# Kernel tuning notes

Measured on AMD Instinct MI355X. Metric: run time of the kernel, lower is better.

Reference implementation:

```python
import jax, jax.numpy as jnp
import numpy as np
import math

B, N = 1, 768
C1, C2 = 384, 128
H, SQK, SV, PQK, PV, NC = 12, 16, 16, 4, 8, 384
EPS = 1e-8
SCALAR_W = math.sqrt(1.0 / (3.0 * SQK))           # sqrt(1/(num_logit_terms*scalar_variance))
POINT_W = math.sqrt(1.0 / (3.0 * (PQK * 9.0 / 2.0)))
W2D = math.sqrt(1.0 / 3.0)


def _quat_to_rot(q):
    # q: [..., 4] -> orthonormal rotation matrices [..., 3, 3]
    q = q / jnp.linalg.norm(q, axis=-1, keepdims=True)
    w, x, y, z = q[..., 0], q[..., 1], q[..., 2], q[..., 3]
    r0 = jnp.stack([1 - 2 * (y * y + z * z), 2 * (x * y - w * z), 2 * (x * z + w * y)], -1)
    r1 = jnp.stack([2 * (x * y + w * z), 1 - 2 * (x * x + z * z), 2 * (y * z - w * x)], -1)
    r2 = jnp.stack([2 * (x * z - w * y), 2 * (y * z + w * x), 1 - 2 * (x * x + y * y)], -1)
    return jnp.stack([r0, r1, r2], -2)


def setup_inputs() -> dict:
    key = jax.random.key(0)
    ks = jax.random.split(key, 12)

    def lin(k, o, i):
        kw, kb = jax.random.split(k)
        w = jax.random.normal(kw, (o, i), jnp.float32) / np.sqrt(i).astype(np.float32)
        b = jax.random.normal(kb, (o,), jnp.float32) * 0.01
        return w, b

    w_qs, b_qs = lin(ks[0], H * SQK, C1)
    w_kvs, b_kvs = lin(ks[1], H * (SV + SQK), C1)
    w_qp, b_qp = lin(ks[2], H * 3 * PQK, C1)
    w_kvp, b_kvp = lin(ks[3], H * 3 * (PQK + PV), C1)
    w_a2, b_a2 = lin(ks[4], H, C2)
    w_o, b_o = lin(ks[5], NC, H * (C2 + SV + 4 * PV))
    return {
        'inputs_1d': jax.random.normal(ks[6], (B, N, C1), jnp.float32),
        'inputs_2d': jax.random.normal(ks[7], (B, N, N, C2), jnp.float32),
        'mask': jnp.ones((B, N, 1), jnp.float32),
        'rotation': _quat_to_rot(jax.random.normal(ks[8], (B, N, 4), jnp.float32)),
        'translation': jax.random.normal(ks[9], (B, N, 3), jnp.float32) * 10.0,
        'w_q_scalar': w_qs, 'b_q_scalar': b_qs,
        'w_kv_scalar': w_kvs, 'b_kv_scalar': b_kvs,
        'w_q_point': w_qp, 'b_q_point': b_qp,
        'w_kv_point': w_kvp, 'b_kv_point': b_kvp,
        'tpw': jnp.ones((H,), jnp.float32),
        'w_attn2d': w_a2, 'b_attn2d': b_a2,
        'w_out': w_o, 'b_out': b_o,
    }


def ipa_forward(inputs_1d, inputs_2d, mask, rotation, translation,
                w_q_scalar, b_q_scalar, w_kv_scalar, b_kv_scalar,
                w_q_point, b_q_point, w_kv_point, b_kv_point,
                tpw, w_attn2d, b_attn2d, w_out, b_out):
    Bs, Ns, _ = inputs_1d.shape

    # scalar q/k/v
    q_scalar = (inputs_1d @ w_q_scalar.T + b_q_scalar).reshape(Bs, Ns, H, SQK)
    kv_scalar = (inputs_1d @ w_kv_scalar.T + b_kv_scalar).reshape(Bs, Ns, H, SQK + SV)
    k_scalar, v_scalar = kv_scalar[..., :SQK], kv_scalar[..., SQK:]

    # point q/k/v in local frame; split order is 3 coord chunks of size H*P
    qp = (inputs_1d @ w_q_point.T + b_q_point).reshape(Bs, Ns, 3, H * PQK)
    kvp = (inputs_1d @ w_kv_point.T + b_kv_point).reshape(Bs, Ns, 3, H * (PQK + PV))
    # to global frame: p_global = R @ p_local + t
    qg = jnp.einsum('bnij,bnjm->bnim', rotation, qp) + translation[..., None]
    kvg = jnp.einsum('bnij,bnjm->bnim', rotation, kvp) + translation[..., None]
    q_point = qg.reshape(Bs, Ns, 3, H, PQK).transpose(0, 3, 1, 4, 2)          # [B,H,N,Pqk,3]
    kv_point = kvg.reshape(Bs, Ns, 3, H, PQK + PV).transpose(0, 3, 1, 4, 2)    # [B,H,N,Pqk+Pv,3]
    k_point, v_point = kv_point[..., :PQK, :], kv_point[..., PQK:, :]

    # point-distance attention term: sum_{p,c} (q-k)^2 = |q|^2 + |k|^2 - 2 q.k
    pw = jax.nn.softplus(tpw) * POINT_W                                       # [H]
    qn = jnp.sum(q_point * q_point, axis=(-1, -2))                             # [B,H,N]
    kn = jnp.sum(k_point * k_point, axis=(-1, -2))
    qk = jnp.einsum('bhipc,bhjpc->bhij', q_point, k_point)
    dist2 = qn[..., :, None] + kn[..., None, :] - 2.0 * qk                     # [B,H,N,N]
    attn_qk_point = -0.5 * pw[None, :, None, None] * dist2

    # scalar attention term
    attn_qk_scalar = jnp.einsum('bihd,bjhd->bhij', SCALAR_W * q_scalar, k_scalar)

    # pair-bias term
    a2d = inputs_2d @ w_attn2d.T + b_attn2d                                    # [B,N,N,H]
    logits = attn_qk_scalar + attn_qk_point + W2D * a2d.transpose(0, 3, 1, 2)

    mask2d = mask * jnp.swapaxes(mask, -1, -2)                                 # [B,N,N]
    logits = logits - 1e5 * (1.0 - mask2d[:, None, :, :])
    attn = jax.nn.softmax(logits, axis=-1)                                     # [B,H,N,N]

    # scalar values
    result_scalar = jnp.einsum('bhij,bjhd->bihd', attn, v_scalar).reshape(Bs, Ns, H * SV)

    # point values (global), then back to local frame: p_local = R^T (p - t)
    rpg = jnp.einsum('bhij,bhjpc->bhipc', attn, v_point)                       # [B,H,N,Pv,3]
    rpg = rpg.transpose(0, 2, 4, 1, 3).reshape(Bs, Ns, 3, H * PV)              # [B,N,3,M]
    local = jnp.einsum('bnji,bnjm->bnim', rotation, rpg - translation[..., None])
    dist = jnp.sqrt(EPS + jnp.sum(local * local, axis=2))                      # [B,N,M]

    # attention over pair features
    r2d = jnp.einsum('bhij,bijc->bihc', attn, inputs_2d).reshape(Bs, Ns, H * C2)

    final_act = jnp.concatenate(
        [result_scalar, local[:, :, 0], local[:, :, 1], local[:, :, 2], dist, r2d], axis=-1)
    return final_act @ w_out.T + b_out


def reference(inputs_1d, inputs_2d, mask, rotation, translation,
              w_q_scalar, b_q_scalar, w_kv_scalar, b_kv_scalar,
              w_q_point, b_q_point, w_kv_point, b_kv_point,
              tpw, w_attn2d, b_attn2d, w_out, b_out):
    return ipa_forward(inputs_1d, inputs_2d, mask, rotation, translation,
                       w_q_scalar, b_q_scalar, w_kv_scalar, b_kv_scalar,
                       w_q_point, b_q_point, w_kv_point, b_kv_point,
                       tpw, w_attn2d, b_attn2d, w_out, b_out)
```

## Files before the change

kernel.cpp:

```cpp
#include <hip/hip_runtime.h>
#include <hip/hip_bf16.h>
#include <math.h>

#define NRES 768
#define C1 384
#define C2 128
#define NH 12

#define OFF_QS   0
#define OFF_KS   147456
#define OFF_VS   294912
#define OFF_QPT  442368
#define OFF_KPT  552960
#define OFF_VPT  663552
#define OFF_FA   884736
#define OFF_RAW  OFF_FA

__device__ __forceinline__ float dot4(float4 a, float4 b) {
    return fmaf(a.x, b.x, fmaf(a.y, b.y, fmaf(a.z, b.z, a.w * b.w)));
}

static constexpr float SCALAR_W = 0.14433756729740643f;
static constexpr float POINT_W  = 0.13608276348795434f;
static constexpr float W2D_W    = 0.57735026918962576f;

__device__ __forceinline__ void wsel(int o,
    const float* w_qs, const float* b_qs, const float* w_kvs, const float* b_kvs,
    const float* w_qp, const float* b_qp, const float* w_kvp, const float* b_kvp,
    const float** row, float* bias)
{
    if (o < 192)      { *row = w_qs  + (size_t)o * C1;         *bias = b_qs[o]; }
    else if (o < 576) { *row = w_kvs + (size_t)(o - 192) * C1; *bias = b_kvs[o - 192]; }
    else if (o < 720) { *row = w_qp  + (size_t)(o - 576) * C1; *bias = b_qp[o - 576]; }
    else              { *row = w_kvp + (size_t)(o - 720) * C1; *bias = b_kvp[o - 720]; }
}

__global__ __launch_bounds__(256) void k1_gemm(
    const float* __restrict__ in1d,
    const float* __restrict__ w_qs, const float* __restrict__ b_qs,
    const float* __restrict__ w_kvs, const float* __restrict__ b_kvs,
    const float* __restrict__ w_qp, const float* __restrict__ b_qp,
    const float* __restrict__ w_kvp, const float* __restrict__ b_kvp,
    float* __restrict__ ws)
{
    __shared__ __align__(16) float ASt[32][68];
    __shared__ __align__(16) float WSt[32][68];
    const int t = threadIdx.x;
    const int n0 = blockIdx.x * 64;
    const int o0 = blockIdx.y * 64;
    const int tx = t & 15, ty = t >> 4;
    float acc[4][4];
    #pragma unroll
    for (int r = 0; r < 4; ++r)
        #pragma unroll
        for (int c = 0; c < 4; ++c) acc[r][c] = 0.f;

    for (int k0 = 0; k0 < C1; k0 += 32) {
        __syncthreads();
        #pragma unroll
        for (int s = 0; s < 2; ++s) {
            int q = t + 256 * s;
            int row = q >> 3, kq = (q & 7) * 4;
            float4 a4 = *(const float4*)&in1d[(size_t)(n0 + row) * C1 + k0 + kq];
            ASt[kq + 0][row] = a4.x; ASt[kq + 1][row] = a4.y;
            ASt[kq + 2][row] = a4.z; ASt[kq + 3][row] = a4.w;
            const float* wr; float bb;
            wsel(o0 + row, w_qs, b_qs, w_kvs, b_kvs, w_qp, b_qp, w_kvp, b_kvp, &wr, &bb);
            float4 w4 = *(const float4*)&wr[k0 + kq];
            WSt[kq + 0][row] = w4.x; WSt[kq + 1][row] = w4.y;
            WSt[kq + 2][row] = w4.z; WSt[kq + 3][row] = w4.w;
        }
        __syncthreads();
        #pragma unroll
        for (int k = 0; k < 32; ++k) {
            float4 a4 = *(const float4*)&ASt[k][ty * 4];
            float4 w4 = *(const float4*)&WSt[k][tx * 4];
            float av[4] = {a4.x, a4.y, a4.z, a4.w};
            float wv[4] = {w4.x, w4.y, w4.z, w4.w};
            #pragma unroll
            for (int r = 0; r < 4; ++r)
                #pragma unroll
                for (int c = 0; c < 4; ++c)
                    acc[r][c] = fmaf(av[r], wv[c], acc[r][c]);
        }
    }
    float bias[4];
    #pragma unroll
    for (int c = 0; c < 4; ++c) {
        const float* dummy;
        wsel(o0 + tx * 4 + c, w_qs, b_qs, w_kvs, b_kvs, w_qp, b_qp, w_kvp, b_kvp, &dummy, &bias[c]);
    }
    float* raw = ws + OFF_RAW;
    #pragma unroll
    for (int r = 0; r < 4; ++r) {
        int n = n0 + ty * 4 + r;
        *(float4*)&raw[(size_t)n * 1152 + o0 + tx * 4] =
            make_float4(acc[r][0] + bias[0], acc[r][1] + bias[1],
                        acc[r][2] + bias[2], acc[r][3] + bias[3]);
    }
}

__global__ __launch_bounds__(256) void k1b_scatter(
    const float* __restrict__ rot, const float* __restrict__ trans,
    float* __restrict__ ws)
{
    __shared__ __align__(16) float rawS[1152];
    const int t = threadIdx.x;
    const int i = blockIdx.x;
    const float* raw = ws + OFF_RAW + (size_t)i * 1152;
    for (int q = t; q < 288; q += 256) *(float4*)&rawS[q * 4] = *(const float4*)&raw[q * 4];
    __syncthreads();
    float* qs  = ws + OFF_QS;  float* ks  = ws + OFF_KS;  float* vs  = ws + OFF_VS;
    float* qpt = ws + OFF_QPT; float* kpt = ws + OFF_KPT; float* vpt = ws + OFF_VPT;

    for (int o = t; o < 576; o += 256) {
        float v = rawS[o];
        if (o < 192) {
            qs[(size_t)i * 192 + o] = v * SCALAR_W;
        } else {
            int idx = o - 192, h = idx >> 5, d = idx & 31;
            if (d < 16) ks[(size_t)i * 192 + h * 16 + d] = v;
            else        vs[(size_t)i * 192 + h * 16 + (d - 16)] = v;
        }
    }
    if (t < 192) {
        int m = t;
        float x0, x1, x2;
        if (m < 48) { x0 = rawS[576 + m]; x1 = rawS[624 + m]; x2 = rawS[672 + m]; }
        else { int mm = m - 48; x0 = rawS[720 + mm]; x1 = rawS[864 + mm]; x2 = rawS[1008 + mm]; }
        float g[3];
        #pragma unroll
        for (int ii = 0; ii < 3; ++ii)
            g[ii] = rot[i * 9 + ii * 3 + 0] * x0 + rot[i * 9 + ii * 3 + 1] * x1 +
                    rot[i * 9 + ii * 3 + 2] * x2 + trans[i * 3 + ii];
        if (m < 48) {
            #pragma unroll
            for (int ii = 0; ii < 3; ++ii) qpt[(size_t)i * 144 + 3 * m + ii] = g[ii];
        } else {
            int mm = m - 48, h = mm / 12, pp = mm % 12;
            if (pp < 4) {
                #pragma unroll
                for (int ii = 0; ii < 3; ++ii) kpt[(size_t)i * 144 + h * 12 + pp * 3 + ii] = g[ii];
            } else {
                #pragma unroll
                for (int ii = 0; ii < 3; ++ii) vpt[(size_t)i * 288 + h * 24 + (pp - 4) * 3 + ii] = g[ii];
            }
        }
    }
}

#define TJ 256
__global__ __launch_bounds__(256) void k2_attn(
    const float* __restrict__ in2d,
    const float* __restrict__ mask,
    const float* __restrict__ rot, const float* __restrict__ trans,
    const float* __restrict__ tpw,
    const float* __restrict__ w2d, const float* __restrict__ b2d,
    float* __restrict__ ws)
{
    __shared__ __align__(16) float P[NH][264];
    __shared__ __align__(16) float tileS[64][128];
    __shared__ __align__(16) float qsS[192];
    __shared__ __align__(16) float qptS[144];
    __shared__ float qnS[NH], phS[NH], bbS[NH], mS[NH], lS[NH], aS[NH];
    __shared__ float rpgS[288];
    const int t = threadIdx.x;
    const int i = blockIdx.x;

    const float* qs  = ws + OFF_QS;  const float* ks  = ws + OFF_KS;  const float* vs = ws + OFF_VS;
    const float* qpt = ws + OFF_QPT; const float* kpt = ws + OFF_KPT; const float* vpt = ws + OFF_VPT;

    if (t < 48) *(float4*)&qsS[t * 4] = *(const float4*)&qs[(size_t)i * 192 + t * 4];
    else if (t >= 64 && t < 100) { int u = t - 64; *(float4*)&qptS[u * 4] = *(const float4*)&qpt[(size_t)i * 144 + u * 4]; }
    __syncthreads();
    if (t < NH) {
        float s = 0.f;
        #pragma unroll
        for (int e = 0; e < 12; ++e) { float x = qptS[t * 12 + e]; s += x * x; }
        qnS[t] = s;
        phS[t] = -0.5f * POINT_W * logf(1.f + __expf(tpw[t]));
        bbS[t] = W2D_W * b2d[t];
        mS[t] = -1e30f;
        lS[t] = 0.f;
    }
    __syncthreads();
    const float mi = mask[i];

    float ra[4] = {0.f, 0.f, 0.f, 0.f};
    float rb[4] = {0.f, 0.f, 0.f, 0.f};
    const bool isR2 = (t < 192);
    int h0 = 0, h1 = 0, c4 = 0, o0 = 0, vh = 0;
    const float* vbase = nullptr; int vstride = 0; bool vact = false;
    if (isR2) { h0 = (t >> 5) * 2; h1 = h0 + 1; c4 = t & 31; }
    else {
        int u = t - 192; o0 = u * 8; vact = (u < 60);
        if (vact) {
            if (o0 < 192) { vh = o0 >> 4; vbase = vs + o0; vstride = 192; }
            else { int q0 = o0 - 192; vh = q0 / 24; vbase = vpt + q0; vstride = 288; }
        }
    }

    for (int tile = 0; tile < 3; ++tile) {
        const int j0 = tile * TJ;
        __syncthreads();
        {
            const int j = j0 + t;
            float acc[NH];
            #pragma unroll
            for (int h = 0; h < NH; ++h) acc[h] = 0.f;
            const float* row = in2d + ((size_t)i * NRES + j) * C2;
            #pragma unroll 8
            for (int cc = 0; cc < 32; ++cc) {
                float4 v4 = *(const float4*)&row[cc * 4];
                #pragma unroll
                for (int h = 0; h < NH; ++h) {
                    float4 w4 = *(const float4*)&w2d[h * C2 + cc * 4];
                    acc[h] += dot4(v4, w4);
                }
            }
            const float msub = -100000.0f * (1.0f - mi * mask[j]);
            const float* ksr  = ks  + (size_t)j * 192;
            const float* kptr = kpt + (size_t)j * 144;
            #pragma unroll
            for (int h = 0; h < NH; ++h) {
                float sq = 0.f;
                #pragma unroll
                for (int d4 = 0; d4 < 4; ++d4) {
                    float4 q4 = *(const float4*)&qsS[h * 16 + d4 * 4];
                    float4 k4 = *(const float4*)&ksr[h * 16 + d4 * 4];
                    sq += dot4(q4, k4);
                }
                float qk = 0.f, kk = 0.f;
                #pragma unroll
                for (int e4 = 0; e4 < 3; ++e4) {
                    float4 qp4 = *(const float4*)&qptS[h * 12 + e4 * 4];
                    float4 kp4 = *(const float4*)&kptr[h * 12 + e4 * 4];
                    qk += dot4(qp4, kp4);
                    kk += dot4(kp4, kp4);
                }
                P[h][t] = sq + phS[h] * (qnS[h] + kk - 2.f * qk) + W2D_W * acc[h] + bbS[h] + msub;
            }
        }
        __syncthreads();
        {
            int wv = t >> 6, lane = t & 63;
            for (int h = wv * 3; h < wv * 3 + 3; ++h) {
                float v0 = P[h][lane], v1 = P[h][lane + 64], v2 = P[h][lane + 128], v3 = P[h][lane + 192];
                float mt = fmaxf(fmaxf(v0, v1), fmaxf(v2, v3));
                #pragma unroll
                for (int off = 32; off > 0; off >>= 1) mt = fmaxf(mt, __shfl_xor(mt, off));
                float mold = mS[h];
                float mnew = fmaxf(mold, mt);
                float e0 = __expf(v0 - mnew), e1 = __expf(v1 - mnew);
                float e2 = __expf(v2 - mnew), e3 = __expf(v3 - mnew);
                P[h][lane] = e0; P[h][lane + 64] = e1; P[h][lane + 128] = e2; P[h][lane + 192] = e3;
                float s = e0 + e1 + e2 + e3;
                #pragma unroll
                for (int off = 32; off > 0; off >>= 1) s += __shfl_xor(s, off);
                if (lane == 0) {
                    float a = __expf(mold - mnew);
                    aS[h] = a;
                    lS[h] = lS[h] * a + s;
                    mS[h] = mnew;
                }
            }
        }
        __syncthreads();
        if (isR2) {
            float a0 = aS[h0], a1 = aS[h1];
            #pragma unroll
            for (int k = 0; k < 4; ++k) { ra[k] *= a0; rb[k] *= a1; }
        } else if (vact) {
            float a = aS[vh];
            #pragma unroll
            for (int k = 0; k < 4; ++k) { ra[k] *= a; rb[k] *= a; }
        }
        for (int sub = 0; sub < 4; ++sub) {
            __syncthreads();
            #pragma unroll
            for (int s = 0; s < 8; ++s) {
                int q = t + 256 * s;
                int rr = q >> 5, cc = q & 31;
                *(float4*)&tileS[rr][cc * 4] =
                    *(const float4*)&in2d[((size_t)i * NRES + j0 + sub * 64 + rr) * C2 + cc * 4];
            }
            __syncthreads();
            if (isR2) {
                for (int jj = 0; jj < 64; jj += 4) {
                    int jt = sub * 64 + jj;
                    float4 p0 = *(const float4*)&P[h0][jt];
                    float4 p1 = *(const float4*)&P[h1][jt];
                    float w0[4] = {p0.x, p0.y, p0.z, p0.w};
                    float w1[4] = {p1.x, p1.y, p1.z, p1.w};
                    #pragma unroll
                    for (int k = 0; k < 4; ++k) {
                        float4 v4 = *(const float4*)&tileS[jj + k][c4 * 4];
                        ra[0] = fmaf(w0[k], v4.x, ra[0]); ra[1] = fmaf(w0[k], v4.y, ra[1]);
                        ra[2] = fmaf(w0[k], v4.z, ra[2]); ra[3] = fmaf(w0[k], v4.w, ra[3]);
                        rb[0] = fmaf(w1[k], v4.x, rb[0]); rb[1] = fmaf(w1[k], v4.y, rb[1]);
                        rb[2] = fmaf(w1[k], v4.z, rb[2]); rb[3] = fmaf(w1[k], v4.w, rb[3]);
                    }
                }
            } else if (vact) {
                for (int jj = 0; jj < 64; jj += 4) {
                    int jt = sub * 64 + jj;
                    int jg = j0 + jt;
                    float4 p = *(const float4*)&P[vh][jt];
                    float w[4] = {p.x, p.y, p.z, p.w};
                    #pragma unroll
                    for (int k = 0; k < 4; ++k) {
                        float4 va = *(const float4*)&vbase[(size_t)(jg + k) * vstride];
                        float4 vb = *(const float4*)&vbase[(size_t)(jg + k) * vstride + 4];
                        ra[0] = fmaf(w[k], va.x, ra[0]); ra[1] = fmaf(w[k], va.y, ra[1]);
                        ra[2] = fmaf(w[k], va.z, ra[2]); ra[3] = fmaf(w[k], va.w, ra[3]);
                        rb[0] = fmaf(w[k], vb.x, rb[0]); rb[1] = fmaf(w[k], vb.y, rb[1]);
                        rb[2] = fmaf(w[k], vb.z, rb[2]); rb[3] = fmaf(w[k], vb.w, rb[3]);
                    }
                }
            }
        }
    }
    float* fa = ws + OFF_FA + (size_t)i * 2112;
    if (isR2) {
        float n0v = 1.f / lS[h0], n1v = 1.f / lS[h1];
        *(float4*)&fa[576 + h0 * 128 + c4 * 4] = make_float4(ra[0] * n0v, ra[1] * n0v, ra[2] * n0v, ra[3] * n0v);
        *(float4*)&fa[576 + h1 * 128 + c4 * 4] = make_float4(rb[0] * n1v, rb[1] * n1v, rb[2] * n1v, rb[3] * n1v);
    } else if (vact) {
        float nv = 1.f / lS[vh];
        if (o0 < 192) {
            *(float4*)&fa[o0]     = make_float4(ra[0] * nv, ra[1] * nv, ra[2] * nv, ra[3] * nv);
            *(float4*)&fa[o0 + 4] = make_float4(rb[0] * nv, rb[1] * nv, rb[2] * nv, rb[3] * nv);
        } else {
            int q0 = o0 - 192;
            *(float4*)&rpgS[q0]     = make_float4(ra[0] * nv, ra[1] * nv, ra[2] * nv, ra[3] * nv);
            *(float4*)&rpgS[q0 + 4] = make_float4(rb[0] * nv, rb[1] * nv, rb[2] * nv, rb[3] * nv);
        }
    }
    __syncthreads();
    if (t < 96) {
        int h = t >> 3, p = t & 7;
        float rv[3];
        #pragma unroll
        for (int c = 0; c < 3; ++c) rv[c] = rpgS[h * 24 + p * 3 + c] - trans[i * 3 + c];
        float l0 = rot[i * 9 + 0] * rv[0] + rot[i * 9 + 3] * rv[1] + rot[i * 9 + 6] * rv[2];
        float l1 = rot[i * 9 + 1] * rv[0] + rot[i * 9 + 4] * rv[1] + rot[i * 9 + 7] * rv[2];
        float l2 = rot[i * 9 + 2] * rv[0] + rot[i * 9 + 5] * rv[1] + rot[i * 9 + 8] * rv[2];
        float dd = sqrtf(1e-8f + l0 * l0 + l1 * l1 + l2 * l2);
        fa[192 + t] = l0;
        fa[288 + t] = l1;
        fa[384 + t] = l2;
        fa[480 + t] = dd;
    }
}

__global__ __launch_bounds__(256) void k3_out(
    const float* __restrict__ w_out, const float* __restrict__ b_out,
    const float* __restrict__ ws, float* __restrict__ out)
{
    __shared__ __align__(16) float ASt[32][34];
    __shared__ __align__(16) float WSt[32][34];
    const int t = threadIdx.x;
    const int i0 = blockIdx.x * 32;
    const int o0 = blockIdx.y * 32;
    const float* fa = ws + OFF_FA;
    int tx = t & 15, ty = t >> 4;
    float acc00 = 0.f, acc01 = 0.f, acc10 = 0.f, acc11 = 0.f;
    int r = t >> 3, kq = (t & 7) * 4;

    for (int k0 = 0; k0 < 2112; k0 += 32) {
        __syncthreads();
        {
            float4 a4 = *(const float4*)&fa[(size_t)(i0 + r) * 2112 + k0 + kq];
            ASt[kq + 0][r] = a4.x; ASt[kq + 1][r] = a4.y; ASt[kq + 2][r] = a4.z; ASt[kq + 3][r] = a4.w;
            float4 w4 = *(const float4*)&w_out[(size_t)(o0 + r) * 2112 + k0 + kq];
            WSt[kq + 0][r] = w4.x; WSt[kq + 1][r] = w4.y; WSt[kq + 2][r] = w4.z; WSt[kq + 3][r] = w4.w;
        }
        __syncthreads();
        #pragma unroll
        for (int k = 0; k < 32; ++k) {
            float2 av = *(const float2*)&ASt[k][ty * 2];
            float2 wv = *(const float2*)&WSt[k][tx * 2];
            acc00 = fmaf(av.x, wv.x, acc00);
            acc01 = fmaf(av.x, wv.y, acc01);
            acc10 = fmaf(av.y, wv.x, acc10);
            acc11 = fmaf(av.y, wv.y, acc11);
        }
    }
    int oi = i0 + ty * 2, oo = o0 + tx * 2;
    out[(size_t)oi * 384 + oo]           = acc00 + b_out[oo];
    out[(size_t)oi * 384 + oo + 1]       = acc01 + b_out[oo + 1];
    out[(size_t)(oi + 1) * 384 + oo]     = acc10 + b_out[oo];
    out[(size_t)(oi + 1) * 384 + oo + 1] = acc11 + b_out[oo + 1];
}

extern "C" void kernel_launch(void* const* d_in, const int* in_sizes, int n_in,
                              void* d_out, int out_size, void* d_ws, size_t ws_size,
                              hipStream_t stream) {
    const float* in1d  = (const float*)d_in[0];
    const float* in2d  = (const float*)d_in[1];
    const float* mask  = (const float*)d_in[2];
    const float* rot   = (const float*)d_in[3];
    const float* trans = (const float*)d_in[4];
    const float* w_qs  = (const float*)d_in[5];
    const float* b_qs  = (const float*)d_in[6];
    const float* w_kvs = (const float*)d_in[7];
    const float* b_kvs = (const float*)d_in[8];
    const float* w_qp  = (const float*)d_in[9];
    const float* b_qp  = (const float*)d_in[10];
    const float* w_kvp = (const float*)d_in[11];
    const float* b_kvp = (const float*)d_in[12];
    const float* tpw   = (const float*)d_in[13];
    const float* w2d   = (const float*)d_in[14];
    const float* b2d   = (const float*)d_in[15];
    const float* w_out = (const float*)d_in[16];
    const float* b_out = (const float*)d_in[17];
    float* ws  = (float*)d_ws;
    float* out = (float*)d_out;

    hipLaunchKernelGGL(k1_gemm, dim3(12, 18), dim3(256), 0, stream,
                       in1d, w_qs, b_qs, w_kvs, b_kvs, w_qp, b_qp, w_kvp, b_kvp, ws);
    hipLaunchKernelGGL(k1b_scatter, dim3(768), dim3(256), 0, stream,
                       rot, trans, ws);
    hipLaunchKernelGGL(k2_attn, dim3(768), dim3(256), 0, stream,
                       in2d, mask, rot, trans, tpw, w2d, b2d, ws);
    hipLaunchKernelGGL(k3_out, dim3(24, 12), dim3(256), 0, stream,
                       w_out, b_out, ws, out);
}
```

Measured before the change: 702.3 us.

## Read pair features once per tile with register prefetch and per-wave softmax

The attention kernel now handles 64-key tiles. Each tile of pair features is loaded into shared memory once and reused for both the 2D logit projection and the weighted pair-feature sum, where before the row was read twice from global memory. The next tile is prefetched into registers while the current one is consumed. Each wave computes logits and the online softmax for three heads, with no separate softmax pass. The output GEMM also gets register double-buffering of its global loads. The cost is more tile iterations and barriers, and a smaller key tile per softmax rescale.

```diff
diff --git a/kernel.cpp b/kernel.cpp
--- a/kernel.cpp
+++ b/kernel.cpp
@@ -149,7 +149,7 @@
     }
 }
 
-#define TJ 256
+#define TJ2 64
 __global__ __launch_bounds__(256) void k2_attn(
     const float* __restrict__ in2d,
     const float* __restrict__ mask,
@@ -158,8 +158,8 @@
     const float* __restrict__ w2d, const float* __restrict__ b2d,
     float* __restrict__ ws)
 {
-    __shared__ __align__(16) float P[NH][264];
-    __shared__ __align__(16) float tileS[64][128];
+    __shared__ __align__(16) float tileS[64][132];
+    __shared__ __align__(16) float P[NH][68];
     __shared__ __align__(16) float qsS[192];
     __shared__ __align__(16) float qptS[144];
     __shared__ float qnS[NH], phS[NH], bbS[NH], mS[NH], lS[NH], aS[NH];
@@ -183,15 +183,16 @@
         mS[t] = -1e30f;
         lS[t] = 0.f;
     }
-    __syncthreads();
     const float mi = mask[i];
 
-    float ra[4] = {0.f, 0.f, 0.f, 0.f};
-    float rb[4] = {0.f, 0.f, 0.f, 0.f};
+    const int jrow = t >> 2, p = t & 3;
+    const int lane = t & 63;
+    const int wv = __builtin_amdgcn_readfirstlane(t >> 6);
+    const int h0w = wv * 3;
     const bool isR2 = (t < 192);
-    int h0 = 0, h1 = 0, c4 = 0, o0 = 0, vh = 0;
+    int h0p = 0, h1p = 0, c4 = 0, o0 = 0, vh = 0;
     const float* vbase = nullptr; int vstride = 0; bool vact = false;
-    if (isR2) { h0 = (t >> 5) * 2; h1 = h0 + 1; c4 = t & 31; }
+    if (isR2) { h0p = (t >> 5) * 2; h1p = h0p + 1; c4 = t & 31; }
     else {
         int u = t - 192; o0 = u * 8; vact = (u < 60);
         if (vact) {
@@ -200,96 +201,90 @@
         }
     }
 
-    for (int tile = 0; tile < 3; ++tile) {
-        const int j0 = tile * TJ;
+    float ra[4] = {0.f, 0.f, 0.f, 0.f};
+    float rb[4] = {0.f, 0.f, 0.f, 0.f};
+
+    float4 r[8];
+    {
+        const float* nr = in2d + ((size_t)i * NRES + jrow) * C2 + p * 32;
+        #pragma unroll
+        for (int k = 0; k < 8; ++k) r[k] = *(const float4*)&nr[k * 4];
+    }
+
+    for (int tile = 0; tile < 12; ++tile) {
+        const int j0 = tile * TJ2;
+        __syncthreads();
+        #pragma unroll
+        for (int k = 0; k < 8; ++k) *(float4*)&tileS[jrow][p * 32 + k * 4] = r[k];
         __syncthreads();
         {
-            const int j = j0 + t;
-            float acc[NH];
+            const int j = j0 + lane;
+            const float* ksr  = ks  + (size_t)j * 192 + h0w * 16;
+            const float* kptr = kpt + (size_t)j * 144 + h0w * 12;
+            const float msub = -100000.0f * (1.0f - mi * mask[j]);
+            const float* wrow = w2d + h0w * C2;
+            float a0 = 0.f, a1 = 0.f, a2 = 0.f;
             #pragma unroll
-            for (int h = 0; h < NH; ++h) acc[h] = 0.f;
-            const float* row = in2d + ((size_t)i * NRES + j) * C2;
-            #pragma unroll 8
-            for (int cc = 0; cc < 32; ++cc) {
-                float4 v4 = *(const float4*)&row[cc * 4];
-                #pragma unroll
-                for (int h = 0; h < NH; ++h) {
-                    float4 w4 = *(const float4*)&w2d[h * C2 + cc * 4];
-                    acc[h] += dot4(v4, w4);
-                }
+            for (int c = 0; c < 32; ++c) {
+                float4 v4 = *(const float4*)&tileS[lane][c * 4];
+                a0 += dot4(v4, *(const float4*)&wrow[c * 4]);
+                a1 += dot4(v4, *(const float4*)&wrow[C2 + c * 4]);
+                a2 += dot4(v4, *(const float4*)&wrow[2 * C2 + c * 4]);
             }
-            const float msub = -100000.0f * (1.0f - mi * mask[j]);
-            const float* ksr  = ks  + (size_t)j * 192;
-            const float* kptr = kpt + (size_t)j * 144;
+            float lg[3];
             #pragma unroll
-            for (int h = 0; h < NH; ++h) {
+            for (int e = 0; e < 3; ++e) {
+                int h = h0w + e;
                 float sq = 0.f;
                 #pragma unroll
-                for (int d4 = 0; d4 < 4; ++d4) {
-                    float4 q4 = *(const float4*)&qsS[h * 16 + d4 * 4];
-                    float4 k4 = *(const float4*)&ksr[h * 16 + d4 * 4];
-                    sq += dot4(q4, k4);
-                }
+                for (int d4 = 0; d4 < 4; ++d4)
+                    sq += dot4(*(const float4*)&qsS[h * 16 + d4 * 4],
+                               *(const float4*)&ksr[e * 16 + d4 * 4]);
                 float qk = 0.f, kk = 0.f;
                 #pragma unroll
                 for (int e4 = 0; e4 < 3; ++e4) {
+                    float4 kp4 = *(const float4*)&kptr[e * 12 + e4 * 4];
                     float4 qp4 = *(const float4*)&qptS[h * 12 + e4 * 4];
-                    float4 kp4 = *(const float4*)&kptr[h * 12 + e4 * 4];
                     qk += dot4(qp4, kp4);
                     kk += dot4(kp4, kp4);
                 }
-                P[h][t] = sq + phS[h] * (qnS[h] + kk - 2.f * qk) + W2D_W * acc[h] + bbS[h] + msub;
+                float a2d = (e == 0) ? a0 : ((e == 1) ? a1 : a2);
+                lg[e] = sq + phS[h] * (qnS[h] + kk - 2.f * qk) + W2D_W * a2d + bbS[h] + msub;
             }
-        }
-        __syncthreads();
-        {
-            int wv = t >> 6, lane = t & 63;
-            for (int h = wv * 3; h < wv * 3 + 3; ++h) {
-                float v0 = P[h][lane], v1 = P[h][lane + 64], v2 = P[h][lane + 128], v3 = P[h][lane + 192];
-                float mt = fmaxf(fmaxf(v0, v1), fmaxf(v2, v3));
+            #pragma unroll
+            for (int e = 0; e < 3; ++e) {
+                int h = h0w + e;
+                float mt = lg[e];
                 #pragma unroll
                 for (int off = 32; off > 0; off >>= 1) mt = fmaxf(mt, __shfl_xor(mt, off));
                 float mold = mS[h];
                 float mnew = fmaxf(mold, mt);
-                float e0 = __expf(v0 - mnew), e1 = __expf(v1 - mnew);
-                float e2 = __expf(v2 - mnew), e3 = __expf(v3 - mnew);
-                P[h][lane] = e0; P[h][lane + 64] = e1; P[h][lane + 128] = e2; P[h][lane + 192] = e3;
-                float s = e0 + e1 + e2 + e3;
+                float ev = __expf(lg[e] - mnew);
+                P[h][lane] = ev;
+                float s = ev;
                 #pragma unroll
                 for (int off = 32; off > 0; off >>= 1) s += __shfl_xor(s, off);
                 if (lane == 0) {
-                    float a = __expf(mold - mnew);
-                    aS[h] = a;
-                    lS[h] = lS[h] * a + s;
+                    float al = __expf(mold - mnew);
+                    aS[h] = al;
+                    lS[h] = lS[h] * al + s;
                     mS[h] = mnew;
                 }
             }
         }
         __syncthreads();
-        if (isR2) {
-            float a0 = aS[h0], a1 = aS[h1];
-            #pragma unroll
-            for (int k = 0; k < 4; ++k) { ra[k] *= a0; rb[k] *= a1; }
-        } else if (vact) {
-            float a = aS[vh];
-            #pragma unroll
-            for (int k = 0; k < 4; ++k) { ra[k] *= a; rb[k] *= a; }
-        }
-        for (int sub = 0; sub < 4; ++sub) {
-            __syncthreads();
-            #pragma unroll
-            for (int s = 0; s < 8; ++s) {
-                int q = t + 256 * s;
-                int rr = q >> 5, cc = q & 31;
-                *(float4*)&tileS[rr][cc * 4] =
-                    *(const float4*)&in2d[((size_t)i * NRES + j0 + sub * 64 + rr) * C2 + cc * 4];
-            }
-            __syncthreads();
+        {
+            int nt = (tile < 11) ? tile + 1 : 11;
+            const float* nr = in2d + ((size_t)i * NRES + nt * TJ2 + jrow) * C2 + p * 32;
             if (isR2) {
+                float al0 = aS[h0p], al1 = aS[h1p];
+                #pragma unroll
+                for (int k = 0; k < 4; ++k) { ra[k] *= al0; rb[k] *= al1; }
+                #pragma unroll
+                for (int k = 0; k < 8; ++k) r[k] = *(const float4*)&nr[k * 4];
                 for (int jj = 0; jj < 64; jj += 4) {
-                    int jt = sub * 64 + jj;
-                    float4 p0 = *(const float4*)&P[h0][jt];
-                    float4 p1 = *(const float4*)&P[h1][jt];
+                    float4 p0 = *(const float4*)&P[h0p][jj];
+                    float4 p1 = *(const float4*)&P[h1p][jj];
                     float w0[4] = {p0.x, p0.y, p0.z, p0.w};
                     float w1[4] = {p1.x, p1.y, p1.z, p1.w};
                     #pragma unroll
@@ -301,20 +296,26 @@
                         rb[2] = fmaf(w1[k], v4.z, rb[2]); rb[3] = fmaf(w1[k], v4.w, rb[3]);
                     }
                 }
-            } else if (vact) {
-                for (int jj = 0; jj < 64; jj += 4) {
-                    int jt = sub * 64 + jj;
-                    int jg = j0 + jt;
-                    float4 p = *(const float4*)&P[vh][jt];
-                    float w[4] = {p.x, p.y, p.z, p.w};
+            } else {
+                #pragma unroll
+                for (int k = 0; k < 8; ++k) r[k] = *(const float4*)&nr[k * 4];
+                if (vact) {
+                    float al = aS[vh];
                     #pragma unroll
-                    for (int k = 0; k < 4; ++k) {
-                        float4 va = *(const float4*)&vbase[(size_t)(jg + k) * vstride];
-                        float4 vb = *(const float4*)&vbase[(size_t)(jg + k) * vstride + 4];
-                        ra[0] = fmaf(w[k], va.x, ra[0]); ra[1] = fmaf(w[k], va.y, ra[1]);
-                        ra[2] = fmaf(w[k], va.z, ra[2]); ra[3] = fmaf(w[k], va.w, ra[3]);
-                        rb[0] = fmaf(w[k], vb.x, rb[0]); rb[1] = fmaf(w[k], vb.y, rb[1]);
-                        rb[2] = fmaf(w[k], vb.z, rb[2]); rb[3] = fmaf(w[k], vb.w, rb[3]);
+                    for (int k = 0; k < 4; ++k) { ra[k] *= al; rb[k] *= al; }
+                    for (int jj = 0; jj < 64; jj += 4) {
+                        int jg = j0 + jj;
+                        float4 pv = *(const float4*)&P[vh][jj];
+                        float w[4] = {pv.x, pv.y, pv.z, pv.w};
+                        #pragma unroll
+                        for (int k = 0; k < 4; ++k) {
+                            float4 va = *(const float4*)&vbase[(size_t)(jg + k) * vstride];
+                            float4 vb = *(const float4*)&vbase[(size_t)(jg + k) * vstride + 4];
+                            ra[0] = fmaf(w[k], va.x, ra[0]); ra[1] = fmaf(w[k], va.y, ra[1]);
+                            ra[2] = fmaf(w[k], va.z, ra[2]); ra[3] = fmaf(w[k], va.w, ra[3]);
+                            rb[0] = fmaf(w[k], vb.x, rb[0]); rb[1] = fmaf(w[k], vb.y, rb[1]);
+                            rb[2] = fmaf(w[k], vb.z, rb[2]); rb[3] = fmaf(w[k], vb.w, rb[3]);
+                        }
                     }
                 }
             }
@@ -322,9 +323,9 @@
     }
     float* fa = ws + OFF_FA + (size_t)i * 2112;
     if (isR2) {
-        float n0v = 1.f / lS[h0], n1v = 1.f / lS[h1];
-        *(float4*)&fa[576 + h0 * 128 + c4 * 4] = make_float4(ra[0] * n0v, ra[1] * n0v, ra[2] * n0v, ra[3] * n0v);
-        *(float4*)&fa[576 + h1 * 128 + c4 * 4] = make_float4(rb[0] * n1v, rb[1] * n1v, rb[2] * n1v, rb[3] * n1v);
+        float n0v = 1.f / lS[h0p], n1v = 1.f / lS[h1p];
+        *(float4*)&fa[576 + h0p * 128 + c4 * 4] = make_float4(ra[0] * n0v, ra[1] * n0v, ra[2] * n0v, ra[3] * n0v);
+        *(float4*)&fa[576 + h1p * 128 + c4 * 4] = make_float4(rb[0] * n1v, rb[1] * n1v, rb[2] * n1v, rb[3] * n1v);
     } else if (vact) {
         float nv = 1.f / lS[vh];
         if (o0 < 192) {
@@ -338,10 +339,10 @@
     }
     __syncthreads();
     if (t < 96) {
-        int h = t >> 3, p = t & 7;
+        int h = t >> 3, pp = t & 7;
         float rv[3];
         #pragma unroll
-        for (int c = 0; c < 3; ++c) rv[c] = rpgS[h * 24 + p * 3 + c] - trans[i * 3 + c];
+        for (int c = 0; c < 3; ++c) rv[c] = rpgS[h * 24 + pp * 3 + c] - trans[i * 3 + c];
         float l0 = rot[i * 9 + 0] * rv[0] + rot[i * 9 + 3] * rv[1] + rot[i * 9 + 6] * rv[2];
         float l1 = rot[i * 9 + 1] * rv[0] + rot[i * 9 + 4] * rv[1] + rot[i * 9 + 7] * rv[2];
         float l2 = rot[i * 9 + 2] * rv[0] + rot[i * 9 + 5] * rv[1] + rot[i * 9 + 8] * rv[2];
@@ -366,16 +367,19 @@
     int tx = t & 15, ty = t >> 4;
     float acc00 = 0.f, acc01 = 0.f, acc10 = 0.f, acc11 = 0.f;
     int r = t >> 3, kq = (t & 7) * 4;
+    const float* arow = fa + (size_t)(i0 + r) * 2112 + kq;
+    const float* wrow = w_out + (size_t)(o0 + r) * 2112 + kq;
+    float4 a4 = *(const float4*)&arow[0];
+    float4 w4 = *(const float4*)&wrow[0];
 
     for (int k0 = 0; k0 < 2112; k0 += 32) {
-        __syncthreads();
-        {
-            float4 a4 = *(const float4*)&fa[(size_t)(i0 + r) * 2112 + k0 + kq];
-            ASt[kq + 0][r] = a4.x; ASt[kq + 1][r] = a4.y; ASt[kq + 2][r] = a4.z; ASt[kq + 3][r] = a4.w;
-            float4 w4 = *(const float4*)&w_out[(size_t)(o0 + r) * 2112 + k0 + kq];
-            WSt[kq + 0][r] = w4.x; WSt[kq + 1][r] = w4.y; WSt[kq + 2][r] = w4.z; WSt[kq + 3][r] = w4.w;
-        }
-        __syncthreads();
+        ASt[kq + 0][r] = a4.x; ASt[kq + 1][r] = a4.y; ASt[kq + 2][r] = a4.z; ASt[kq + 3][r] = a4.w;
+        WSt[kq + 0][r] = w4.x; WSt[kq + 1][r] = w4.y; WSt[kq + 2][r] = w4.z; WSt[kq + 3][r] = w4.w;
+        __syncthreads();
+        if (k0 + 32 < 2112) {
+            a4 = *(const float4*)&arow[k0 + 32];
+            w4 = *(const float4*)&wrow[k0 + 32];
+        }
         #pragma unroll
         for (int k = 0; k < 32; ++k) {
             float2 av = *(const float2*)&ASt[k][ty * 2];
@@ -385,6 +389,7 @@
             acc10 = fmaf(av.y, wv.x, acc10);
             acc11 = fmaf(av.y, wv.y, acc11);
         }
+        __syncthreads();
     }
     int oi = i0 + ty * 2, oo = o0 + tx * 2;
     out[(size_t)oi * 384 + oo]           = acc00 + b_out[oo];
```

Measured after the change: 972.6 us. 38.5% more time.

## Restructure attention kernel to full-row softmax with 512 threads and split-j accumulation

Applied to the files above, without the earlier changes.

The attention kernel now launches 512 threads and computes logits for all 768 keys up front. It replaces the online (tiled) softmax with a single full-row softmax, so the running max and rescale bookkeeping disappears. Accumulation splits each row across two half-waves over j and combines them with a shuffle. The output GEMM kernel adds register prefetch of the next K tile to overlap global loads with compute. Shared memory for the logits grows, which may limit occupancy.

```diff
diff --git a/kernel.cpp b/kernel.cpp
--- a/kernel.cpp
+++ b/kernel.cpp
@@ -149,8 +149,7 @@
     }
 }
 
-#define TJ 256
-__global__ __launch_bounds__(256) void k2_attn(
+__global__ __launch_bounds__(512, 4) void k2_attn(
     const float* __restrict__ in2d,
     const float* __restrict__ mask,
     const float* __restrict__ rot, const float* __restrict__ trans,
@@ -158,14 +157,16 @@
     const float* __restrict__ w2d, const float* __restrict__ b2d,
     float* __restrict__ ws)
 {
-    __shared__ __align__(16) float P[NH][264];
-    __shared__ __align__(16) float tileS[64][128];
+    __shared__ __align__(16) float P[NH][776];
+    __shared__ __align__(16) float tileS[32][132];
     __shared__ __align__(16) float qsS[192];
     __shared__ __align__(16) float qptS[144];
-    __shared__ float qnS[NH], phS[NH], bbS[NH], mS[NH], lS[NH], aS[NH];
+    __shared__ float qnS[NH], phS[NH], bbS[NH];
     __shared__ float rpgS[288];
     const int t = threadIdx.x;
     const int i = blockIdx.x;
+    const int lane = t & 63;
+    const int wv = t >> 6;
 
     const float* qs  = ws + OFF_QS;  const float* ks  = ws + OFF_KS;  const float* vs = ws + OFF_VS;
     const float* qpt = ws + OFF_QPT; const float* kpt = ws + OFF_KPT; const float* vpt = ws + OFF_VPT;
@@ -180,168 +181,158 @@
         qnS[t] = s;
         phS[t] = -0.5f * POINT_W * logf(1.f + __expf(tpw[t]));
         bbS[t] = W2D_W * b2d[t];
-        mS[t] = -1e30f;
-        lS[t] = 0.f;
     }
     __syncthreads();
     const float mi = mask[i];
 
+    for (int j = t; j < NRES; j += 512) {
+        float acc[NH];
+        #pragma unroll
+        for (int h = 0; h < NH; ++h) acc[h] = 0.f;
+        const float* row = in2d + ((size_t)i * NRES + j) * C2;
+        #pragma unroll 8
+        for (int cc = 0; cc < 32; ++cc) {
+            float4 v4 = *(const float4*)&row[cc * 4];
+            #pragma unroll
+            for (int h = 0; h < NH; ++h) {
+                float4 w4 = *(const float4*)&w2d[h * C2 + cc * 4];
+                acc[h] += dot4(v4, w4);
+            }
+        }
+        const float msub = -100000.0f * (1.0f - mi * mask[j]);
+        const float* ksr  = ks  + (size_t)j * 192;
+        const float* kptr = kpt + (size_t)j * 144;
+        #pragma unroll
+        for (int h = 0; h < NH; ++h) {
+            float sq = 0.f;
+            #pragma unroll
+            for (int d4 = 0; d4 < 4; ++d4) {
+                float4 q4 = *(const float4*)&qsS[h * 16 + d4 * 4];
+                float4 k4 = *(const float4*)&ksr[h * 16 + d4 * 4];
+                sq += dot4(q4, k4);
+            }
+            float qk = 0.f, kk = 0.f;
+            #pragma unroll
+            for (int e4 = 0; e4 < 3; ++e4) {
+                float4 qp4 = *(const float4*)&qptS[h * 12 + e4 * 4];
+                float4 kp4 = *(const float4*)&kptr[h * 12 + e4 * 4];
+                qk += dot4(qp4, kp4);
+                kk += dot4(kp4, kp4);
+            }
+            P[h][j] = sq + phS[h] * (qnS[h] + kk - 2.f * qk) + W2D_W * acc[h] + bbS[h] + msub;
+        }
+    }
+    __syncthreads();
+
+    for (int h = wv; h < NH; h += 8) {
+        float v[12];
+        float mx = -1e30f;
+        #pragma unroll
+        for (int k = 0; k < 12; ++k) { v[k] = P[h][lane + 64 * k]; mx = fmaxf(mx, v[k]); }
+        #pragma unroll
+        for (int off = 32; off > 0; off >>= 1) mx = fmaxf(mx, __shfl_xor(mx, off));
+        float s = 0.f;
+        #pragma unroll
+        for (int k = 0; k < 12; ++k) { v[k] = __expf(v[k] - mx); s += v[k]; }
+        #pragma unroll
+        for (int off = 32; off > 0; off >>= 1) s += __shfl_xor(s, off);
+        float rinv = 1.0f / s;
+        #pragma unroll
+        for (int k = 0; k < 12; ++k) P[h][lane + 64 * k] = v[k] * rinv;
+    }
+    __syncthreads();
+
+    const int jh = lane >> 5;
+    const int c4 = lane & 31;
     float ra[4] = {0.f, 0.f, 0.f, 0.f};
     float rb[4] = {0.f, 0.f, 0.f, 0.f};
-    const bool isR2 = (t < 192);
-    int h0 = 0, h1 = 0, c4 = 0, o0 = 0, vh = 0;
+    int h0 = 0, h1 = 0, vh = 0, vo0 = 0;
     const float* vbase = nullptr; int vstride = 0; bool vact = false;
-    if (isR2) { h0 = (t >> 5) * 2; h1 = h0 + 1; c4 = t & 31; }
+    if (wv < 6) { h0 = wv * 2; h1 = h0 + 1; }
     else {
-        int u = t - 192; o0 = u * 8; vact = (u < 60);
+        int l = lane & 31;
+        vact = (l < 30);
+        vo0 = 240 * (wv - 6) + l * 8;
         if (vact) {
-            if (o0 < 192) { vh = o0 >> 4; vbase = vs + o0; vstride = 192; }
-            else { int q0 = o0 - 192; vh = q0 / 24; vbase = vpt + q0; vstride = 288; }
-        }
-    }
-
-    for (int tile = 0; tile < 3; ++tile) {
-        const int j0 = tile * TJ;
+            if (vo0 < 192) { vh = vo0 >> 4; vbase = vs + vo0; vstride = 192; }
+            else { int q0 = vo0 - 192; vh = q0 / 24; vbase = vpt + q0; vstride = 288; }
+        }
+    }
+
+    for (int sub = 0; sub < 24; ++sub) {
         __syncthreads();
         {
-            const int j = j0 + t;
-            float acc[NH];
-            #pragma unroll
-            for (int h = 0; h < NH; ++h) acc[h] = 0.f;
-            const float* row = in2d + ((size_t)i * NRES + j) * C2;
-            #pragma unroll 8
-            for (int cc = 0; cc < 32; ++cc) {
-                float4 v4 = *(const float4*)&row[cc * 4];
+            int rr = t >> 4, cq = (t & 15) * 8;
+            const float* src = &in2d[((size_t)i * NRES + sub * 32 + rr) * C2 + cq];
+            float4 x0 = *(const float4*)&src[0];
+            float4 x1 = *(const float4*)&src[4];
+            *(float4*)&tileS[rr][cq] = x0;
+            *(float4*)&tileS[rr][cq + 4] = x1;
+        }
+        __syncthreads();
+        const int jbase = sub * 32 + jh * 16;
+        const int jloc = jh * 16;
+        if (wv < 6) {
+            #pragma unroll
+            for (int jj = 0; jj < 16; jj += 4) {
+                float4 p0 = *(const float4*)&P[h0][jbase + jj];
+                float4 p1 = *(const float4*)&P[h1][jbase + jj];
+                float w0[4] = {p0.x, p0.y, p0.z, p0.w};
+                float w1[4] = {p1.x, p1.y, p1.z, p1.w};
                 #pragma unroll
-                for (int h = 0; h < NH; ++h) {
-                    float4 w4 = *(const float4*)&w2d[h * C2 + cc * 4];
-                    acc[h] += dot4(v4, w4);
+                for (int k = 0; k < 4; ++k) {
+                    float4 v4 = *(const float4*)&tileS[jloc + jj + k][c4 * 4];
+                    ra[0] = fmaf(w0[k], v4.x, ra[0]); ra[1] = fmaf(w0[k], v4.y, ra[1]);
+                    ra[2] = fmaf(w0[k], v4.z, ra[2]); ra[3] = fmaf(w0[k], v4.w, ra[3]);
+                    rb[0] = fmaf(w1[k], v4.x, rb[0]); rb[1] = fmaf(w1[k], v4.y, rb[1]);
+                    rb[2] = fmaf(w1[k], v4.z, rb[2]); rb[3] = fmaf(w1[k], v4.w, rb[3]);
                 }
             }
-            const float msub = -100000.0f * (1.0f - mi * mask[j]);
-            const float* ksr  = ks  + (size_t)j * 192;
-            const float* kptr = kpt + (size_t)j * 144;
-            #pragma unroll
-            for (int h = 0; h < NH; ++h) {
-                float sq = 0.f;
+        } else if (vact) {
+            #pragma unroll
+            for (int jj = 0; jj < 16; jj += 4) {
+                float4 pv = *(const float4*)&P[vh][jbase + jj];
+                float w[4] = {pv.x, pv.y, pv.z, pv.w};
                 #pragma unroll
-                for (int d4 = 0; d4 < 4; ++d4) {
-                    float4 q4 = *(const float4*)&qsS[h * 16 + d4 * 4];
-                    float4 k4 = *(const float4*)&ksr[h * 16 + d4 * 4];
-                    sq += dot4(q4, k4);
+                for (int k = 0; k < 4; ++k) {
+                    float4 va = *(const float4*)&vbase[(size_t)(jbase + jj + k) * vstride];
+                    float4 vb = *(const float4*)&vbase[(size_t)(jbase + jj + k) * vstride + 4];
+                    ra[0] = fmaf(w[k], va.x, ra[0]); ra[1] = fmaf(w[k], va.y, ra[1]);
+                    ra[2] = fmaf(w[k], va.z, ra[2]); ra[3] = fmaf(w[k], va.w, ra[3]);
+                    rb[0] = fmaf(w[k], vb.x, rb[0]); rb[1] = fmaf(w[k], vb.y, rb[1]);
+                    rb[2] = fmaf(w[k], vb.z, rb[2]); rb[3] = fmaf(w[k], vb.w, rb[3]);
                 }
-                float qk = 0.f, kk = 0.f;
-                #pragma unroll
-                for (int e4 = 0; e4 < 3; ++e4) {
-                    float4 qp4 = *(const float4*)&qptS[h * 12 + e4 * 4];
-                    float4 kp4 = *(const float4*)&kptr[h * 12 + e4 * 4];
-                    qk += dot4(qp4, kp4);
-                    kk += dot4(kp4, kp4);
-                }
-                P[h][t] = sq + phS[h] * (qnS[h] + kk - 2.f * qk) + W2D_W * acc[h] + bbS[h] + msub;
-            }
-        }
-        __syncthreads();
-        {
-            int wv = t >> 6, lane = t & 63;
-            for (int h = wv * 3; h < wv * 3 + 3; ++h) {
-                float v0 = P[h][lane], v1 = P[h][lane + 64], v2 = P[h][lane + 128], v3 = P[h][lane + 192];
-                float mt = fmaxf(fmaxf(v0, v1), fmaxf(v2, v3));
-                #pragma unroll
-                for (int off = 32; off > 0; off >>= 1) mt = fmaxf(mt, __shfl_xor(mt, off));
-                float mold = mS[h];
-                float mnew = fmaxf(mold, mt);
-                float e0 = __expf(v0 - mnew), e1 = __expf(v1 - mnew);
-                float e2 = __expf(v2 - mnew), e3 = __expf(v3 - mnew);
-                P[h][lane] = e0; P[h][lane + 64] = e1; P[h][lane + 128] = e2; P[h][lane + 192] = e3;
-                float s = e0 + e1 + e2 + e3;
-                #pragma unroll
-                for (int off = 32; off > 0; off >>= 1) s += __shfl_xor(s, off);
-                if (lane == 0) {
-                    float a = __expf(mold - mnew);
-                    aS[h] = a;
-                    lS[h] = lS[h] * a + s;
-                    mS[h] = mnew;
-                }
-            }
-        }
-        __syncthreads();
-        if (isR2) {
-            float a0 = aS[h0], a1 = aS[h1];
-            #pragma unroll
-            for (int k = 0; k < 4; ++k) { ra[k] *= a0; rb[k] *= a1; }
-        } else if (vact) {
-            float a = aS[vh];
-            #pragma unroll
-            for (int k = 0; k < 4; ++k) { ra[k] *= a; rb[k] *= a; }
-        }
-        for (int sub = 0; sub < 4; ++sub) {
-            __syncthreads();
-            #pragma unroll
-            for (int s = 0; s < 8; ++s) {
-                int q = t + 256 * s;
-                int rr = q >> 5, cc = q & 31;
-                *(float4*)&tileS[rr][cc * 4] =
-                    *(const float4*)&in2d[((size_t)i * NRES + j0 + sub * 64 + rr) * C2 + cc * 4];
-            }
-            __syncthreads();
-            if (isR2) {
-                for (int jj = 0; jj < 64; jj += 4) {
-                    int jt = sub * 64 + jj;
-                    float4 p0 = *(const float4*)&P[h0][jt];
-                    float4 p1 = *(const float4*)&P[h1][jt];
-                    float w0[4] = {p0.x, p0.y, p0.z, p0.w};
-                    float w1[4] = {p1.x, p1.y, p1.z, p1.w};
-                    #pragma unroll
-                    for (int k = 0; k < 4; ++k) {
-                        float4 v4 = *(const float4*)&tileS[jj + k][c4 * 4];
-                        ra[0] = fmaf(w0[k], v4.x, ra[0]); ra[1] = fmaf(w0[k], v4.y, ra[1]);
-                        ra[2] = fmaf(w0[k], v4.z, ra[2]); ra[3] = fmaf(w0[k], v4.w, ra[3]);
-                        rb[0] = fmaf(w1[k], v4.x, rb[0]); rb[1] = fmaf(w1[k], v4.y, rb[1]);
-                        rb[2] = fmaf(w1[k], v4.z, rb[2]); rb[3] = fmaf(w1[k], v4.w, rb[3]);
-                    }
-                }
-            } else if (vact) {
-                for (int jj = 0; jj < 64; jj += 4) {
-                    int jt = sub * 64 + jj;
-                    int jg = j0 + jt;
-                    float4 p = *(const float4*)&P[vh][jt];
-                    float w[4] = {p.x, p.y, p.z, p.w};
-                    #pragma unroll
-                    for (int k = 0; k < 4; ++k) {
-                        float4 va = *(const float4*)&vbase[(size_t)(jg + k) * vstride];
-                        float4 vb = *(const float4*)&vbase[(size_t)(jg + k) * vstride + 4];
-                        ra[0] = fmaf(w[k], va.x, ra[0]); ra[1] = fmaf(w[k], va.y, ra[1]);
-                        ra[2] = fmaf(w[k], va.z, ra[2]); ra[3] = fmaf(w[k], va.w, ra[3]);
-                        rb[0] = fmaf(w[k], vb.x, rb[0]); rb[1] = fmaf(w[k], vb.y, rb[1]);
-                        rb[2] = fmaf(w[k], vb.z, rb[2]); rb[3] = fmaf(w[k], vb.w, rb[3]);
-                    }
-                }
-            }
-        }
-    }
+            }
+        }
+    }
+
     float* fa = ws + OFF_FA + (size_t)i * 2112;
-    if (isR2) {
-        float n0v = 1.f / lS[h0], n1v = 1.f / lS[h1];
-        *(float4*)&fa[576 + h0 * 128 + c4 * 4] = make_float4(ra[0] * n0v, ra[1] * n0v, ra[2] * n0v, ra[3] * n0v);
-        *(float4*)&fa[576 + h1 * 128 + c4 * 4] = make_float4(rb[0] * n1v, rb[1] * n1v, rb[2] * n1v, rb[3] * n1v);
-    } else if (vact) {
-        float nv = 1.f / lS[vh];
-        if (o0 < 192) {
-            *(float4*)&fa[o0]     = make_float4(ra[0] * nv, ra[1] * nv, ra[2] * nv, ra[3] * nv);
-            *(float4*)&fa[o0 + 4] = make_float4(rb[0] * nv, rb[1] * nv, rb[2] * nv, rb[3] * nv);
+    #pragma unroll
+    for (int k = 0; k < 4; ++k) {
+        ra[k] += __shfl_xor(ra[k], 32);
+        rb[k] += __shfl_xor(rb[k], 32);
+    }
+    if (wv < 6) {
+        if (lane < 32)
+            *(float4*)&fa[576 + h0 * 128 + c4 * 4] = make_float4(ra[0], ra[1], ra[2], ra[3]);
+        else
+            *(float4*)&fa[576 + h1 * 128 + c4 * 4] = make_float4(rb[0], rb[1], rb[2], rb[3]);
+    } else if (vact && lane < 32) {
+        if (vo0 < 192) {
+            *(float4*)&fa[vo0]     = make_float4(ra[0], ra[1], ra[2], ra[3]);
+            *(float4*)&fa[vo0 + 4] = make_float4(rb[0], rb[1], rb[2], rb[3]);
         } else {
-            int q0 = o0 - 192;
-            *(float4*)&rpgS[q0]     = make_float4(ra[0] * nv, ra[1] * nv, ra[2] * nv, ra[3] * nv);
-            *(float4*)&rpgS[q0 + 4] = make_float4(rb[0] * nv, rb[1] * nv, rb[2] * nv, rb[3] * nv);
+            int q0 = vo0 - 192;
+            *(float4*)&rpgS[q0]     = make_float4(ra[0], ra[1], ra[2], ra[3]);
+            *(float4*)&rpgS[q0 + 4] = make_float4(rb[0], rb[1], rb[2], rb[3]);
         }
     }
     __syncthreads();
     if (t < 96) {
-        int h = t >> 3, p = t & 7;
+        int h = t >> 3, pp = t & 7;
         float rv[3];
         #pragma unroll
-        for (int c = 0; c < 3; ++c) rv[c] = rpgS[h * 24 + p * 3 + c] - trans[i * 3 + c];
+        for (int c = 0; c < 3; ++c) rv[c] = rpgS[h * 24 + pp * 3 + c] - trans[i * 3 + c];
         float l0 = rot[i * 9 + 0] * rv[0] + rot[i * 9 + 3] * rv[1] + rot[i * 9 + 6] * rv[2];
         float l1 = rot[i * 9 + 1] * rv[0] + rot[i * 9 + 4] * rv[1] + rot[i * 9 + 7] * rv[2];
         float l2 = rot[i * 9 + 2] * rv[0] + rot[i * 9 + 5] * rv[1] + rot[i * 9 + 8] * rv[2];
@@ -366,16 +357,19 @@
     int tx = t & 15, ty = t >> 4;
     float acc00 = 0.f, acc01 = 0.f, acc10 = 0.f, acc11 = 0.f;
     int r = t >> 3, kq = (t & 7) * 4;
+    const float* arow = fa + (size_t)(i0 + r) * 2112 + kq;
+    const float* wrow = w_out + (size_t)(o0 + r) * 2112 + kq;
+    float4 a4 = *(const float4*)&arow[0];
+    float4 w4 = *(const float4*)&wrow[0];
 
     for (int k0 = 0; k0 < 2112; k0 += 32) {
-        __syncthreads();
-        {
-            float4 a4 = *(const float4*)&fa[(size_t)(i0 + r) * 2112 + k0 + kq];
-            ASt[kq + 0][r] = a4.x; ASt[kq + 1][r] = a4.y; ASt[kq + 2][r] = a4.z; ASt[kq + 3][r] = a4.w;
-            float4 w4 = *(const float4*)&w_out[(size_t)(o0 + r) * 2112 + k0 + kq];
-            WSt[kq + 0][r] = w4.x; WSt[kq + 1][r] = w4.y; WSt[kq + 2][r] = w4.z; WSt[kq + 3][r] = w4.w;
-        }
-        __syncthreads();
+        ASt[kq + 0][r] = a4.x; ASt[kq + 1][r] = a4.y; ASt[kq + 2][r] = a4.z; ASt[kq + 3][r] = a4.w;
+        WSt[kq + 0][r] = w4.x; WSt[kq + 1][r] = w4.y; WSt[kq + 2][r] = w4.z; WSt[kq + 3][r] = w4.w;
+        __syncthreads();
+        if (k0 + 32 < 2112) {
+            a4 = *(const float4*)&arow[k0 + 32];
+            w4 = *(const float4*)&wrow[k0 + 32];
+        }
         #pragma unroll
         for (int k = 0; k < 32; ++k) {
             float2 av = *(const float2*)&ASt[k][ty * 2];
@@ -385,6 +379,7 @@
             acc10 = fmaf(av.y, wv.x, acc10);
             acc11 = fmaf(av.y, wv.y, acc11);
         }
+        __syncthreads();
     }
     int oi = i0 + ty * 2, oo = o0 + tx * 2;
     out[(size_t)oi * 384 + oo]           = acc00 + b_out[oo];
@@ -421,7 +416,7 @@
                        in1d, w_qs, b_qs, w_kvs, b_kvs, w_qp, b_qp, w_kvp, b_kvp, ws);
     hipLaunchKernelGGL(k1b_scatter, dim3(768), dim3(256), 0, stream,
                        rot, trans, ws);
-    hipLaunchKernelGGL(k2_attn, dim3(768), dim3(256), 0, stream,
+    hipLaunchKernelGGL(k2_attn, dim3(768), dim3(512), 0, stream,
                        in2d, mask, rot, trans, tpw, w2d, b2d, ws);
     hipLaunchKernelGGL(k3_out, dim3(24, 12), dim3(256), 0, stream,
                        w_out, b_out, ws, out);
```

New measurement: 998.8 us. +42.2%, slower.
